# Kernel optimization log

Measured on AMD Instinct MI355X. Metric: run time of the kernel, lower is better.

## Reference

```python
import jax, jax.numpy as jnp
import numpy as np

B, LQ, LK, D_WORD, D_K, D_V = 8, 2048, 2048, 1024, 128, 128
TEMPERATURE = 11.313708498984761  # sqrt(d_k)
NEG_BIG = -1e9


def setup_inputs() -> dict:
    key = jax.random.key(0)
    ks = jax.random.split(key, 7)
    scale = 1.0 / np.sqrt(D_WORD)
    return {
        "q": jax.random.normal(ks[0], (B, LQ, D_WORD), dtype=jnp.float32),
        "k": jax.random.normal(ks[1], (B, LK, D_WORD), dtype=jnp.float32),
        "v": jax.random.normal(ks[2], (B, LK, D_WORD), dtype=jnp.float32),
        "memory_lengths": jax.random.randint(ks[3], (B,), 1, LK + 1, dtype=jnp.int32),
        "Wq": jax.random.normal(ks[4], (D_WORD, D_K), dtype=jnp.float32) * scale,
        "Wk": jax.random.normal(ks[5], (D_WORD, D_K), dtype=jnp.float32) * scale,
        "Wv": jax.random.normal(ks[6], (D_WORD, D_V), dtype=jnp.float32) * scale,
    }


def reference(q, k, v, memory_lengths, Wq, Wk, Wv):
    # Projections (bias-free Dense layers)
    qs = jnp.einsum("bqw,wd->bqd", q, Wq)   # [B, LQ, D_K]
    ks = jnp.einsum("bkw,wd->bkd", k, Wk)   # [B, LK, D_K]
    vs = jnp.einsum("bkw,wd->bkd", v, Wv)   # [B, LK, D_V]
    # Scaled dot-product scores
    attn = jnp.einsum("bqd,bkd->bqk", qs, ks) / TEMPERATURE  # [B, LQ, LK]
    # Padding mask from memory_lengths (tf.sequence_mask + tile + where)
    mem_mask = jnp.arange(attn.shape[-1])[None, None, :] < memory_lengths[:, None, None]
    attn = jnp.where(mem_mask, attn, NEG_BIG)
    p = jax.nn.softmax(attn, axis=-1)
    return jnp.einsum("bqk,bkd->bqd", p, vs)  # [B, LQ, D_V]
```

## Files before the change

kernel.cpp:

```cpp
#include <hip/hip_runtime.h>

typedef _Float16 half8 __attribute__((ext_vector_type(8)));
typedef float floatx4 __attribute__((ext_vector_type(4)));

#define INV_TEMP 0.08838834764831845f

#define OFF_WT   0
#define OFF_QS   786432
#define OFF_KT   (786432 + 4194304)
#define OFF_VT   (OFF_KT + 4194304)
#define OFF_PART (OFF_VT + 4194304)
#define PART_BYTES (2ull * 8 * 2048 * 132 * 4)

__global__ __launch_bounds__(256) void wprep_kernel(
    const float* __restrict__ Wq, const float* __restrict__ Wk,
    const float* __restrict__ Wv, _Float16* __restrict__ wt)
{
    __shared__ _Float16 T[64 * 136];
    const int t = threadIdx.x;
    const int kt = blockIdx.x;
    const int m = blockIdx.y;
    const float* W = (m == 0) ? Wq : (m == 1) ? Wk : Wv;
    const float scale = (m == 0) ? INV_TEMP : 1.0f;
    const float* src = W + kt * 8192;

    #pragma unroll
    for (int i = 0; i < 8; i++) {
        int f = i * 1024 + t * 4;
        float4 v = *(const float4*)(src + f);
        int k = f >> 7, n = f & 127;
        _Float16* d = T + k * 136 + n;
        d[0] = (_Float16)(v.x * scale);
        d[1] = (_Float16)(v.y * scale);
        d[2] = (_Float16)(v.z * scale);
        d[3] = (_Float16)(v.w * scale);
    }
    __syncthreads();

    _Float16* dst = wt + m * 131072 + kt * 8192;
    #pragma unroll
    for (int i = 0; i < 4; i++) {
        int p = i * 256 + t;
        int n = p >> 3;
        int c = (p & 7) ^ (n & 7);
        half8 h;
        #pragma unroll
        for (int j = 0; j < 8; j++)
            h[j] = T[(c * 8 + j) * 136 + n];
        *(half8*)(dst + p * 8) = h;
    }
}

__global__ __launch_bounds__(256) void proj_kernel(
    const float* __restrict__ Xq, const float* __restrict__ Xk,
    const float* __restrict__ Xv, const _Float16* __restrict__ wt,
    _Float16* __restrict__ qs, _Float16* __restrict__ ks_t,
    _Float16* __restrict__ vt_t)
{
    __shared__ float As[2][64 * 64];
    __shared__ _Float16 Bs[2][8192];

    const int t = threadIdx.x;
    const int lane = t & 63;
    const int w = t >> 6;
    const int quad = lane >> 4;
    const int m16 = lane & 15;
    const int yb = blockIdx.y;
    const float* X = (yb == 0) ? Xq : (yb == 1) ? Xk : Xv;
    const _Float16* W = wt + yb * 131072;
    const int m0 = blockIdx.x * 64;

    floatx4 acc[8] = {};
    const int e = m16 & 7;

    auto stage = [&](int buf, int s) {
        {
            const float* base = X + (size_t)m0 * 1024 + s * 64;
            #pragma unroll
            for (int i = 0; i < 4; i++) {
                int st = i * 256 + t;
                int row = st >> 4;
                int p = st & 15;
                int c = (p & 8) | ((p & 7) ^ (row & 7));
                __builtin_amdgcn_global_load_lds(
                    (const __attribute__((address_space(1))) unsigned int*)(base + (size_t)row * 1024 + c * 4),
                    (__attribute__((address_space(3))) unsigned int*)(&As[buf][st * 4]),
                    16, 0, 0);
            }
        }
        {
            const _Float16* src = W + s * 8192;
            #pragma unroll
            for (int i = 0; i < 4; i++) {
                int slot = (w * 4 + i) * 64 + lane;
                __builtin_amdgcn_global_load_lds(
                    (const __attribute__((address_space(1))) unsigned int*)(src + (size_t)slot * 8),
                    (__attribute__((address_space(3))) unsigned int*)(&Bs[buf][slot * 8]),
                    16, 0, 0);
            }
        }
    };

    stage(0, 0);

    for (int s = 0; s < 16; s++) {
        const int cur = s & 1;
        if (s + 1 < 16) {
            stage(cur ^ 1, s + 1);
            asm volatile("s_waitcnt vmcnt(8)" ::: "memory");
        } else {
            asm volatile("s_waitcnt vmcnt(0)" ::: "memory");
        }
        __builtin_amdgcn_s_barrier();
        asm volatile("" ::: "memory");

        const float* ap = &As[cur][(w * 16 + m16) * 64];
        const char* bt = (const char*)&Bs[cur][0];
        #pragma unroll
        for (int hf2 = 0; hf2 < 2; hf2++) {
            float4 fa = *(const float4*)(ap + (hf2 * 8 + ((quad * 2) ^ e)) * 4);
            float4 fb = *(const float4*)(ap + (hf2 * 8 + ((quad * 2 + 1) ^ e)) * 4);
            half8 af = {(_Float16)fa.x, (_Float16)fa.y, (_Float16)fa.z, (_Float16)fa.w,
                        (_Float16)fb.x, (_Float16)fb.y, (_Float16)fb.z, (_Float16)fb.w};
            int sw = (hf2 * 4 + quad) ^ e;
            #pragma unroll
            for (int nt = 0; nt < 8; nt++) {
                half8 bf = *(const half8*)(bt + (nt * 16 + m16) * 128 + sw * 16);
                acc[nt] = __builtin_amdgcn_mfma_f32_16x16x32_f16(af, bf, acc[nt], 0, 0, 0);
            }
        }

        asm volatile("" ::: "memory");
        __builtin_amdgcn_s_barrier();
        asm volatile("" ::: "memory");
    }

    const int b = m0 >> 11;
    const int kt = (m0 & 2047) >> 6;

    if (yb == 0) {
        #pragma unroll
        for (int nt = 0; nt < 8; nt++) {
            #pragma unroll
            for (int r = 0; r < 4; r++) {
                int orow = m0 + w * 16 + quad * 4 + r;
                qs[(size_t)orow * 128 + nt * 16 + m16] = (_Float16)acc[nt][r];
            }
        }
    } else if (yb == 1) {
        _Float16* tile = ks_t + (size_t)(b * 32 + kt) * 8192;
        #pragma unroll
        for (int nt = 0; nt < 8; nt++) {
            #pragma unroll
            for (int r = 0; r < 4; r++) {
                int row = w * 16 + quad * 4 + r;
                int col = nt * 16 + m16;
                int p = row * 16 + ((col >> 3) ^ (row & 7));
                tile[p * 8 + (col & 7)] = (_Float16)acc[nt][r];
            }
        }
    } else {
        __syncthreads();
        _Float16* T = (_Float16*)As;
        #pragma unroll
        for (int nt = 0; nt < 8; nt++) {
            #pragma unroll
            for (int r = 0; r < 4; r++)
                T[(w * 16 + quad * 4 + r) * 130 + nt * 16 + m16] = (_Float16)acc[nt][r];
        }
        __syncthreads();
        int dv = t >> 1, hf = t & 1;
        _Float16* tile = vt_t + (size_t)(b * 32 + kt) * 8192;
        #pragma unroll
        for (int j8 = 0; j8 < 4; j8++) {
            int k8 = hf * 4 + j8;
            half8 h;
            #pragma unroll
            for (int j = 0; j < 8; j++)
                h[j] = T[(k8 * 8 + j) * 130 + dv];
            int p = dv * 8 + (k8 ^ (dv & 7));
            *(half8*)(tile + p * 8) = h;
        }
    }
}

__global__ __launch_bounds__(256) void attn_kernel(
    const _Float16* __restrict__ qs, const _Float16* __restrict__ ks_t,
    const _Float16* __restrict__ vt_t, const int* __restrict__ mlen,
    float* __restrict__ out, float* __restrict__ part, int ns)
{
    __shared__ _Float16 kbuf[2 * 8192];
    __shared__ _Float16 vbuf[2 * 8192];
    __shared__ _Float16 pls[4 * 16 * 72];

    const int t = threadIdx.x;
    const int lane = t & 63;
    const int w = t >> 6;
    const int quad = lane >> 4;
    const int m16 = lane & 15;
    const int b = blockIdx.y;
    const int h = blockIdx.z;
    const int q0 = blockIdx.x * 64;
    const int ml = mlen[b];
    const int nkt = (ml + 63) >> 6;
    const int hs = (nkt + ns - 1) / ns;
    const int kb0 = h * hs;
    const int kb1 = min(nkt, (h + 1) * hs);

    half8 aq[4];
    {
        const _Float16* qrow =
            qs + (size_t)(b * 2048 + q0 + w * 16 + m16) * 128 + quad * 8;
        #pragma unroll
        for (int d = 0; d < 4; d++)
            aq[d] = *(const half8*)(qrow + d * 32);
    }

    floatx4 acc[8] = {};
    float m_i[4] = {-3e38f, -3e38f, -3e38f, -3e38f};
    float l_i[4] = {0.f, 0.f, 0.f, 0.f};

    auto stage = [&](int buf, int kt) {
        const _Float16* ksrc = ks_t + (size_t)(b * 32 + kt) * 8192;
        const _Float16* vsrc = vt_t + (size_t)(b * 32 + kt) * 8192;
        #pragma unroll
        for (int i = 0; i < 4; i++) {
            int slot = (w * 4 + i) * 64 + lane;
            __builtin_amdgcn_global_load_lds(
                (const __attribute__((address_space(1))) unsigned int*)(ksrc + (size_t)slot * 8),
                (__attribute__((address_space(3))) unsigned int*)(kbuf + buf * 8192 + slot * 8),
                16, 0, 0);
            __builtin_amdgcn_global_load_lds(
                (const __attribute__((address_space(1))) unsigned int*)(vsrc + (size_t)slot * 8),
                (__attribute__((address_space(3))) unsigned int*)(vbuf + buf * 8192 + slot * 8),
                16, 0, 0);
        }
    };

    if (kb0 < kb1) {
        stage(0, kb0);
        __builtin_amdgcn_s_waitcnt(0);
        __syncthreads();

        for (int kt = kb0; kt < kb1; kt++) {
            const int cur = (kt - kb0) & 1;
            if (kt + 1 < kb1) stage(cur ^ 1, kt + 1);

            const _Float16* kb = kbuf + cur * 8192;
            const _Float16* vb = vbuf + cur * 8192;
            const int k0 = kt * 64;

            floatx4 sacc[4] = {};
            #pragma unroll
            for (int d = 0; d < 4; d++) {
                #pragma unroll
                for (int nt = 0; nt < 4; nt++) {
                    int row = nt * 16 + m16;
                    int p = row * 16 + ((d * 4 + quad) ^ (row & 7));
                    half8 bf = *(const half8*)(kb + p * 8);
                    sacc[nt] = __builtin_amdgcn_mfma_f32_16x16x32_f16(aq[d], bf, sacc[nt], 0, 0, 0);
                }
            }

            float p4[4][4];
            float rowmax[4], rowsum[4];
            #pragma unroll
            for (int r = 0; r < 4; r++) rowmax[r] = -3e38f;
            #pragma unroll
            for (int nt = 0; nt < 4; nt++) {
                int key = k0 + nt * 16 + m16;
                bool valid = key < ml;
                #pragma unroll
                for (int r = 0; r < 4; r++) {
                    float s = valid ? sacc[nt][r] : -3e38f;
                    p4[nt][r] = s;
                    rowmax[r] = fmaxf(rowmax[r], s);
                }
            }
            #pragma unroll
            for (int mask = 8; mask >= 1; mask >>= 1) {
                #pragma unroll
                for (int r = 0; r < 4; r++)
                    rowmax[r] = fmaxf(rowmax[r], __shfl_xor(rowmax[r], mask, 64));
            }
            #pragma unroll
            for (int r = 0; r < 4; r++) {
                float mnew = fmaxf(m_i[r], rowmax[r]);
                float alpha = __expf(m_i[r] - mnew);
                m_i[r] = mnew;
                l_i[r] *= alpha;
                #pragma unroll
                for (int nt = 0; nt < 8; nt++) acc[nt][r] *= alpha;
                rowsum[r] = 0.f;
                #pragma unroll
                for (int nt = 0; nt < 4; nt++) {
                    float ee = __expf(p4[nt][r] - mnew);
                    p4[nt][r] = ee;
                    rowsum[r] += ee;
                }
            }
            #pragma unroll
            for (int mask = 8; mask >= 1; mask >>= 1) {
                #pragma unroll
                for (int r = 0; r < 4; r++)
                    rowsum[r] += __shfl_xor(rowsum[r], mask, 64);
            }
            #pragma unroll
            for (int r = 0; r < 4; r++) l_i[r] += rowsum[r];

            _Float16* pw = pls + w * 16 * 72;
            #pragma unroll
            for (int nt = 0; nt < 4; nt++) {
                #pragma unroll
                for (int r = 0; r < 4; r++)
                    pw[(quad * 4 + r) * 72 + nt * 16 + m16] = (_Float16)p4[nt][r];
            }

            #pragma unroll
            for (int kp = 0; kp < 2; kp++) {
                half8 pa = *(const half8*)(pw + m16 * 72 + kp * 32 + quad * 8);
                #pragma unroll
                for (int nt = 0; nt < 8; nt++) {
                    int dv = nt * 16 + m16;
                    int p = dv * 8 + ((kp * 4 + quad) ^ (dv & 7));
                    half8 bf = *(const half8*)(vb + p * 8);
                    acc[nt] = __builtin_amdgcn_mfma_f32_16x16x32_f16(pa, bf, acc[nt], 0, 0, 0);
                }
            }

            __builtin_amdgcn_s_waitcnt(0);
            __syncthreads();
        }
    }

    if (ns == 1) {
        #pragma unroll
        for (int r = 0; r < 4; r++) {
            float inv_l = 1.0f / l_i[r];
            int orow = b * 2048 + q0 + w * 16 + quad * 4 + r;
            float* dst = out + (size_t)orow * 128;
            #pragma unroll
            for (int nt = 0; nt < 8; nt++)
                dst[nt * 16 + m16] = acc[nt][r] * inv_l;
        }
    } else {
        #pragma unroll
        for (int r = 0; r < 4; r++) {
            float* pr = part +
                (size_t)(h * 16384 + b * 2048 + q0 + w * 16 + quad * 4 + r) * 132;
            #pragma unroll
            for (int nt = 0; nt < 8; nt++)
                pr[nt * 16 + m16] = acc[nt][r];
            if (m16 == 0) { pr[128] = m_i[r]; pr[129] = l_i[r]; }
        }
    }
}

__global__ __launch_bounds__(256) void merge_kernel(
    const float* __restrict__ part, float* __restrict__ out)
{
    int idx = blockIdx.x * 256 + threadIdx.x;
    int row = idx >> 7, c = idx & 127;
    const float* p1 = part + (size_t)row * 132;
    const float* p2 = part + (size_t)(16384 + row) * 132;
    float m1 = p1[128], l1 = p1[129];
    float m2 = p2[128], l2 = p2[129];
    float M = fmaxf(m1, m2);
    float s1 = __expf(m1 - M), s2 = __expf(m2 - M);
    out[idx] = (p1[c] * s1 + p2[c] * s2) / (l1 * s1 + l2 * s2);
}

extern "C" void kernel_launch(void* const* d_in, const int* in_sizes, int n_in,
                              void* d_out, int out_size, void* d_ws, size_t ws_size,
                              hipStream_t stream) {
    const float* q   = (const float*)d_in[0];
    const float* k   = (const float*)d_in[1];
    const float* v   = (const float*)d_in[2];
    const int* mlen  = (const int*)d_in[3];
    const float* Wq  = (const float*)d_in[4];
    const float* Wk  = (const float*)d_in[5];
    const float* Wv  = (const float*)d_in[6];
    float* out = (float*)d_out;

    char* ws = (char*)d_ws;
    _Float16* wt   = (_Float16*)(ws + OFF_WT);
    _Float16* qs   = (_Float16*)(ws + OFF_QS);
    _Float16* ks_t = (_Float16*)(ws + OFF_KT);
    _Float16* vt_t = (_Float16*)(ws + OFF_VT);
    float* part    = (float*)(ws + OFF_PART);

    const int ns = (ws_size >= (size_t)OFF_PART + PART_BYTES) ? 2 : 1;

    hipLaunchKernelGGL(wprep_kernel, dim3(16, 3), dim3(256), 0, stream, Wq, Wk, Wv, wt);
    hipLaunchKernelGGL(proj_kernel, dim3(256, 3), dim3(256), 0, stream,
                       q, k, v, wt, qs, ks_t, vt_t);
    hipLaunchKernelGGL(attn_kernel, dim3(32, 8, ns), dim3(256), 0, stream,
                       qs, ks_t, vt_t, mlen, out, part, ns);
    if (ns == 2)
        hipLaunchKernelGGL(merge_kernel, dim3(8192), dim3(256), 0, stream, part, out);
}
```

Baseline: 264.2 us.

## Enlarge projection tile to 128 rows and single-buffer the A stage

The projection kernel now computes 128 output rows per block instead of 64, so each wave holds two M-tiles and every B fragment read from LDS feeds two MFMAs. This halves how often the weight tile is reloaded per output row and halves the grid. To stay within 64KB of LDS, the fp32 A tile is single-buffered: its next stage is issued only after the compute barrier, while B stays double-buffered. The trade-off is fewer blocks (384) on the GPU and less overlap between loading A and computing on it.

```diff
diff --git a/kernel.cpp b/kernel.cpp
--- a/kernel.cpp
+++ b/kernel.cpp
@@ -51,14 +51,16 @@
     }
 }
 
-__global__ __launch_bounds__(256) void proj_kernel(
+__global__ __launch_bounds__(256, 2) void proj_kernel(
     const float* __restrict__ Xq, const float* __restrict__ Xk,
     const float* __restrict__ Xv, const _Float16* __restrict__ wt,
     _Float16* __restrict__ qs, _Float16* __restrict__ ks_t,
     _Float16* __restrict__ vt_t)
 {
-    __shared__ float As[2][64 * 64];
-    __shared__ _Float16 Bs[2][8192];
+    __shared__ char smem[65536];
+    float* As = (float*)smem;
+    _Float16* Bs0 = (_Float16*)(smem + 32768);
+    _Float16* Bs1 = (_Float16*)(smem + 49152);
 
     const int t = threadIdx.x;
     const int lane = t & 63;
@@ -68,118 +70,144 @@
     const int yb = blockIdx.y;
     const float* X = (yb == 0) ? Xq : (yb == 1) ? Xk : Xv;
     const _Float16* W = wt + yb * 131072;
-    const int m0 = blockIdx.x * 64;
-
-    floatx4 acc[8] = {};
+    const int m0 = blockIdx.x * 128;
+
+    floatx4 acc[2][8] = {};
     const int e = m16 & 7;
 
-    auto stage = [&](int buf, int s) {
-        {
-            const float* base = X + (size_t)m0 * 1024 + s * 64;
-            #pragma unroll
-            for (int i = 0; i < 4; i++) {
-                int st = i * 256 + t;
-                int row = st >> 4;
-                int p = st & 15;
-                int c = (p & 8) | ((p & 7) ^ (row & 7));
-                __builtin_amdgcn_global_load_lds(
-                    (const __attribute__((address_space(1))) unsigned int*)(base + (size_t)row * 1024 + c * 4),
-                    (__attribute__((address_space(3))) unsigned int*)(&As[buf][st * 4]),
-                    16, 0, 0);
-            }
-        }
-        {
-            const _Float16* src = W + s * 8192;
-            #pragma unroll
-            for (int i = 0; i < 4; i++) {
-                int slot = (w * 4 + i) * 64 + lane;
-                __builtin_amdgcn_global_load_lds(
-                    (const __attribute__((address_space(1))) unsigned int*)(src + (size_t)slot * 8),
-                    (__attribute__((address_space(3))) unsigned int*)(&Bs[buf][slot * 8]),
-                    16, 0, 0);
-            }
-        }
-    };
-
-    stage(0, 0);
+    const float* Xbase = X + (size_t)m0 * 1024;
+
+#define STAGEA(s)                                                             \
+    {                                                                         \
+        _Pragma("unroll")                                                     \
+        for (int _i = 0; _i < 8; _i++) {                                      \
+            int _st = _i * 256 + t;                                           \
+            int _row = _st >> 4;                                              \
+            int _p = _st & 15;                                                \
+            int _c = (_p & 8) | ((_p & 7) ^ (_row & 7));                      \
+            __builtin_amdgcn_global_load_lds(                                 \
+                (const __attribute__((address_space(1))) unsigned int*)(Xbase + (size_t)_row * 1024 + (s) * 64 + _c * 4), \
+                (__attribute__((address_space(3))) unsigned int*)(As + _st * 4), \
+                16, 0, 0);                                                    \
+        }                                                                     \
+    }
+
+#define STAGEB(dst, s)                                                        \
+    {                                                                         \
+        const _Float16* _src = W + (s) * 8192;                                \
+        _Pragma("unroll")                                                     \
+        for (int _i = 0; _i < 4; _i++) {                                      \
+            int _slot = (w * 4 + _i) * 64 + lane;                             \
+            __builtin_amdgcn_global_load_lds(                                 \
+                (const __attribute__((address_space(1))) unsigned int*)(_src + (size_t)_slot * 8), \
+                (__attribute__((address_space(3))) unsigned int*)((dst) + _slot * 8), \
+                16, 0, 0);                                                    \
+        }                                                                     \
+    }
+
+    STAGEA(0);
+    STAGEB(Bs0, 0);
 
     for (int s = 0; s < 16; s++) {
-        const int cur = s & 1;
+        __syncthreads();
+
+        const _Float16* bcur = (s & 1) ? Bs1 : Bs0;
         if (s + 1 < 16) {
-            stage(cur ^ 1, s + 1);
-            asm volatile("s_waitcnt vmcnt(8)" ::: "memory");
-        } else {
-            asm volatile("s_waitcnt vmcnt(0)" ::: "memory");
-        }
+            if (s & 1) { STAGEB(Bs0, s + 1); } else { STAGEB(Bs1, s + 1); }
+        }
+
+        #pragma unroll
+        for (int hf2 = 0; hf2 < 2; hf2++) {
+            half8 af0, af1;
+            #pragma unroll
+            for (int mt = 0; mt < 2; mt++) {
+                int rm = w * 32 + mt * 16 + m16;
+                const float* ap = As + rm * 64;
+                float4 fa = *(const float4*)(ap + (hf2 * 8 + ((quad * 2) ^ e)) * 4);
+                float4 fb = *(const float4*)(ap + (hf2 * 8 + ((quad * 2 + 1) ^ e)) * 4);
+                half8 af = {(_Float16)fa.x, (_Float16)fa.y, (_Float16)fa.z, (_Float16)fa.w,
+                            (_Float16)fb.x, (_Float16)fb.y, (_Float16)fb.z, (_Float16)fb.w};
+                if (mt == 0) af0 = af; else af1 = af;
+            }
+            int sw = (hf2 * 4 + quad) ^ e;
+            #pragma unroll
+            for (int nt = 0; nt < 8; nt++) {
+                half8 bf = *(const half8*)((const char*)bcur + (nt * 16 + m16) * 128 + sw * 16);
+                acc[0][nt] = __builtin_amdgcn_mfma_f32_16x16x32_f16(af0, bf, acc[0][nt], 0, 0, 0);
+                acc[1][nt] = __builtin_amdgcn_mfma_f32_16x16x32_f16(af1, bf, acc[1][nt], 0, 0, 0);
+            }
+        }
+
+        asm volatile("s_waitcnt lgkmcnt(0)" ::: "memory");
         __builtin_amdgcn_s_barrier();
         asm volatile("" ::: "memory");
 
-        const float* ap = &As[cur][(w * 16 + m16) * 64];
-        const char* bt = (const char*)&Bs[cur][0];
-        #pragma unroll
-        for (int hf2 = 0; hf2 < 2; hf2++) {
-            float4 fa = *(const float4*)(ap + (hf2 * 8 + ((quad * 2) ^ e)) * 4);
-            float4 fb = *(const float4*)(ap + (hf2 * 8 + ((quad * 2 + 1) ^ e)) * 4);
-            half8 af = {(_Float16)fa.x, (_Float16)fa.y, (_Float16)fa.z, (_Float16)fa.w,
-                        (_Float16)fb.x, (_Float16)fb.y, (_Float16)fb.z, (_Float16)fb.w};
-            int sw = (hf2 * 4 + quad) ^ e;
+        if (s + 1 < 16) STAGEA(s + 1);
+    }
+
+#undef STAGEA
+#undef STAGEB
+
+    const int b = m0 >> 11;
+    const int kt0 = (m0 & 2047) >> 6;
+
+    if (yb == 0) {
+        #pragma unroll
+        for (int mt = 0; mt < 2; mt++) {
             #pragma unroll
             for (int nt = 0; nt < 8; nt++) {
-                half8 bf = *(const half8*)(bt + (nt * 16 + m16) * 128 + sw * 16);
-                acc[nt] = __builtin_amdgcn_mfma_f32_16x16x32_f16(af, bf, acc[nt], 0, 0, 0);
-            }
-        }
-
-        asm volatile("" ::: "memory");
-        __builtin_amdgcn_s_barrier();
-        asm volatile("" ::: "memory");
-    }
-
-    const int b = m0 >> 11;
-    const int kt = (m0 & 2047) >> 6;
-
-    if (yb == 0) {
-        #pragma unroll
-        for (int nt = 0; nt < 8; nt++) {
-            #pragma unroll
-            for (int r = 0; r < 4; r++) {
-                int orow = m0 + w * 16 + quad * 4 + r;
-                qs[(size_t)orow * 128 + nt * 16 + m16] = (_Float16)acc[nt][r];
+                #pragma unroll
+                for (int r = 0; r < 4; r++) {
+                    int orow = m0 + w * 32 + mt * 16 + quad * 4 + r;
+                    qs[(size_t)orow * 128 + nt * 16 + m16] = (_Float16)acc[mt][nt][r];
+                }
             }
         }
     } else if (yb == 1) {
-        _Float16* tile = ks_t + (size_t)(b * 32 + kt) * 8192;
-        #pragma unroll
-        for (int nt = 0; nt < 8; nt++) {
-            #pragma unroll
-            for (int r = 0; r < 4; r++) {
-                int row = w * 16 + quad * 4 + r;
-                int col = nt * 16 + m16;
-                int p = row * 16 + ((col >> 3) ^ (row & 7));
-                tile[p * 8 + (col & 7)] = (_Float16)acc[nt][r];
+        #pragma unroll
+        for (int mt = 0; mt < 2; mt++) {
+            #pragma unroll
+            for (int nt = 0; nt < 8; nt++) {
+                #pragma unroll
+                for (int r = 0; r < 4; r++) {
+                    int rb = w * 32 + mt * 16 + quad * 4 + r;
+                    int kt = kt0 + (rb >> 6);
+                    int row = rb & 63;
+                    int col = nt * 16 + m16;
+                    _Float16* tile = ks_t + (size_t)(b * 32 + kt) * 8192;
+                    int p = row * 16 + ((col >> 3) ^ (row & 7));
+                    tile[p * 8 + (col & 7)] = (_Float16)acc[mt][nt][r];
+                }
             }
         }
     } else {
-        __syncthreads();
-        _Float16* T = (_Float16*)As;
-        #pragma unroll
-        for (int nt = 0; nt < 8; nt++) {
-            #pragma unroll
-            for (int r = 0; r < 4; r++)
-                T[(w * 16 + quad * 4 + r) * 130 + nt * 16 + m16] = (_Float16)acc[nt][r];
+        _Float16* T = (_Float16*)smem;
+        #pragma unroll
+        for (int mt = 0; mt < 2; mt++) {
+            #pragma unroll
+            for (int nt = 0; nt < 8; nt++) {
+                #pragma unroll
+                for (int r = 0; r < 4; r++) {
+                    int rb = w * 32 + mt * 16 + quad * 4 + r;
+                    T[rb * 130 + nt * 16 + m16] = (_Float16)acc[mt][nt][r];
+                }
+            }
         }
         __syncthreads();
         int dv = t >> 1, hf = t & 1;
-        _Float16* tile = vt_t + (size_t)(b * 32 + kt) * 8192;
-        #pragma unroll
-        for (int j8 = 0; j8 < 4; j8++) {
-            int k8 = hf * 4 + j8;
-            half8 h;
-            #pragma unroll
-            for (int j = 0; j < 8; j++)
-                h[j] = T[(k8 * 8 + j) * 130 + dv];
-            int p = dv * 8 + (k8 ^ (dv & 7));
-            *(half8*)(tile + p * 8) = h;
+        #pragma unroll
+        for (int tile_i = 0; tile_i < 2; tile_i++) {
+            _Float16* tile = vt_t + (size_t)(b * 32 + kt0 + tile_i) * 8192;
+            #pragma unroll
+            for (int j8 = 0; j8 < 4; j8++) {
+                int k8 = hf * 4 + j8;
+                half8 h;
+                #pragma unroll
+                for (int j = 0; j < 8; j++)
+                    h[j] = T[(tile_i * 64 + k8 * 8 + j) * 130 + dv];
+                int p = dv * 8 + (k8 ^ (dv & 7));
+                *(half8*)(tile + p * 8) = h;
+            }
         }
     }
 }
@@ -392,7 +420,7 @@
     const int ns = (ws_size >= (size_t)OFF_PART + PART_BYTES) ? 2 : 1;
 
     hipLaunchKernelGGL(wprep_kernel, dim3(16, 3), dim3(256), 0, stream, Wq, Wk, Wv, wt);
-    hipLaunchKernelGGL(proj_kernel, dim3(256, 3), dim3(256), 0, stream,
+    hipLaunchKernelGGL(proj_kernel, dim3(128, 3), dim3(256), 0, stream,
                        q, k, v, wt, qs, ks_t, vt_t);
     hipLaunchKernelGGL(attn_kernel, dim3(32, 8, ns), dim3(256), 0, stream,
                        qs, ks_t, vt_t, mlen, out, part, ns);
```

Measured after the change: 267.2 us. About the same (+1.2%).
